# Optimization experiments

Hardware: AMD Instinct MI355X
Metric: run time of the kernel (lower is better)

Reference implementation:

```python
import jax, jax.numpy as jnp
import numpy as np

DIM = 128
HID = 128
EPS = 1e-5  # torch LayerNorm default

def _ln(x, g, b):
    mu = jnp.mean(x, axis=-1, keepdims=True)
    var = jnp.mean(jnp.square(x - mu), axis=-1, keepdims=True)
    return (x - mu) * jax.lax.rsqrt(var + EPS) * g + b

def setup_inputs() -> dict:
    key = jax.random.key(0)
    ks = jax.random.split(key, 20)
    B, N = 4, 256
    s_in = 1.0 / np.sqrt(DIM)
    s_hid = 1.0 / np.sqrt(HID)
    inp = {
        "x": jax.random.normal(ks[0], (B, N, N, DIM), jnp.float32),
        "norm_g": jnp.ones((DIM,), jnp.float32),
        "norm_b": jnp.zeros((DIM,), jnp.float32),
        "w_left": jax.random.normal(ks[1], (DIM, HID), jnp.float32) * s_in,
        "b_left": jnp.zeros((HID,), jnp.float32),
        "w_right": jax.random.normal(ks[2], (DIM, HID), jnp.float32) * s_in,
        "b_right": jnp.zeros((HID,), jnp.float32),
        # gates: module inits weight=0, bias=1; use small random weights + bias=1
        # so gradients are non-degenerate while staying near the trained-init regime
        "w_lgate": jax.random.normal(ks[3], (DIM, HID), jnp.float32) * (0.02 * s_in),
        "b_lgate": jnp.ones((HID,), jnp.float32),
        "w_rgate": jax.random.normal(ks[4], (DIM, HID), jnp.float32) * (0.02 * s_in),
        "b_rgate": jnp.ones((HID,), jnp.float32),
        "w_ogate": jax.random.normal(ks[5], (DIM, HID), jnp.float32) * (0.02 * s_in),
        "b_ogate": jnp.ones((HID,), jnp.float32),
        "onorm_g": jnp.ones((HID,), jnp.float32),
        "onorm_b": jnp.zeros((HID,), jnp.float32),
        "w_out": jax.random.normal(ks[6], (HID, DIM), jnp.float32) * s_hid,
        "b_out": jnp.zeros((DIM,), jnp.float32),
    }
    return inp

def reference(x, norm_g, norm_b, w_left, b_left, w_right, b_right,
              w_lgate, b_lgate, w_rgate, b_rgate, w_ogate, b_ogate,
              onorm_g, onorm_b, w_out, b_out):
    # x: [B, N, N, DIM]
    xn = _ln(x, norm_g, norm_b)
    left = (xn @ w_left + b_left) * jax.nn.sigmoid(xn @ w_lgate + b_lgate)
    right = (xn @ w_right + b_right) * jax.nn.sigmoid(xn @ w_rgate + b_rgate)
    out_gate = jax.nn.sigmoid(xn @ w_ogate + b_ogate)
    # 'ingoing' mix: out[b,i,j,d] = sum_k left[b,k,j,d] * right[b,k,i,d]
    mixed = jnp.einsum('bkjd,bkid->bijd', left, right)
    out = _ln(mixed, onorm_g, onorm_b) * out_gate
    return out @ w_out + b_out
```

## Files before the change

### kernel.cpp

```cpp
#include <hip/hip_runtime.h>
#include <hip/hip_fp16.h>

typedef unsigned short u16;
typedef unsigned int   u32;
typedef __attribute__((ext_vector_type(8))) short short8;
typedef __attribute__((ext_vector_type(4))) float f32x4;

#define NN 256
#define DD 128

__device__ __forceinline__ u16 f2b(float f) {
    union { float f; u32 i; } v; v.f = f;
    u32 x = v.i;
    return (u16)((x + 0x7FFFu + ((x >> 16) & 1u)) >> 16);
}
__device__ __forceinline__ float b2f(u16 u) {
    union { u32 i; float f; } v; v.i = ((u32)u) << 16; return v.f;
}
__device__ __forceinline__ u32 cvtpk(float lo, float hi) {
    u32 r;
    asm("v_cvt_pk_bf16_f32 %0, %1, %2" : "=v"(r) : "v"(lo), "v"(hi));
    return r;
}
__device__ __forceinline__ float sigm(float z) { return 1.f / (1.f + __expf(-z)); }

__global__ void k_tw(const float* w0, const float* w1, const float* w2,
                     const float* w3, const float* w4, const float* w5,
                     u16* __restrict__ out) {
    int t = blockIdx.x * 256 + threadIdx.x;
    int mat = t >> 11, idx = t & 2047;
    int lane = idx & 63;
    int s    = (idx >> 6) & 3;
    int nt   = idx >> 8;
    int m = lane & 15, quad = lane >> 4;
    int h  = nt * 16 + m;
    int d0 = s * 32 + quad * 8;
    const float* src = (mat == 0) ? w0 : (mat == 1) ? w1 : (mat == 2) ? w2
                      : (mat == 3) ? w3 : (mat == 4) ? w4 : w5;
    u16 vals[8];
#pragma unroll
    for (int j = 0; j < 8; ++j) vals[j] = f2b(src[(d0 + j) * 128 + h]);
    *(uint4*)(out + (t << 3)) = *(uint4*)vals;
}

__global__ __launch_bounds__(256, 4)
void k_lngemm(const float* __restrict__ x,
              const float* __restrict__ ng,  const float* __restrict__ nb,
              const u16*   __restrict__ wT,
              const float* __restrict__ bL,  const float* __restrict__ bLG,
              const float* __restrict__ bR,  const float* __restrict__ bRG,
              const float* __restrict__ bOG,
              u16* __restrict__ lT, u16* __restrict__ rT, float* __restrict__ og)
{
    __shared__ uint4 smem4[128 * 16];
    uint4*  xs  = smem4;
    __half* ogb = (__half*)smem4;

    const int tid = threadIdx.x;
    const int bx  = blockIdx.x;
    const int b   = bx >> 9;
    const int q   = (bx >> 1) & 255;
    const int p0  = (bx & 1) * 128;

    {
        const int lr = tid >> 4;
        const int c  = tid & 15;
        float gg[8], bbv[8];
        {
            float4 g0 = *(const float4*)(ng + c * 8);
            float4 g1 = *(const float4*)(ng + c * 8 + 4);
            float4 b0 = *(const float4*)(nb + c * 8);
            float4 b1 = *(const float4*)(nb + c * 8 + 4);
            gg[0]=g0.x; gg[1]=g0.y; gg[2]=g0.z; gg[3]=g0.w;
            gg[4]=g1.x; gg[5]=g1.y; gg[6]=g1.z; gg[7]=g1.w;
            bbv[0]=b0.x; bbv[1]=b0.y; bbv[2]=b0.z; bbv[3]=b0.w;
            bbv[4]=b1.x; bbv[5]=b1.y; bbv[6]=b1.z; bbv[7]=b1.w;
        }
#pragma unroll
        for (int pass = 0; pass < 8; ++pass) {
            const int r = pass * 16 + lr;
            const long gRow = (long)((b * NN + p0 + r) * NN + q);
            float4 x0 = *(const float4*)(x + gRow * DD + c * 8);
            float4 x1 = *(const float4*)(x + gRow * DD + c * 8 + 4);
            float f[8] = {x0.x, x0.y, x0.z, x0.w, x1.x, x1.y, x1.z, x1.w};
            float s1 = 0.f, s2 = 0.f;
#pragma unroll
            for (int j = 0; j < 8; ++j) { s1 += f[j]; s2 += f[j] * f[j]; }
#pragma unroll
            for (int off = 1; off < 16; off <<= 1) {
                s1 += __shfl_xor(s1, off);
                s2 += __shfl_xor(s2, off);
            }
            const float mu = s1 * (1.f / 128.f);
            const float rs = rsqrtf(s2 * (1.f / 128.f) - mu * mu + 1e-5f);
            uint4 pk;
            pk.x = cvtpk((f[0]-mu)*rs*gg[0]+bbv[0], (f[1]-mu)*rs*gg[1]+bbv[1]);
            pk.y = cvtpk((f[2]-mu)*rs*gg[2]+bbv[2], (f[3]-mu)*rs*gg[3]+bbv[3]);
            pk.z = cvtpk((f[4]-mu)*rs*gg[4]+bbv[4], (f[5]-mu)*rs*gg[5]+bbv[5]);
            pk.w = cvtpk((f[6]-mu)*rs*gg[6]+bbv[6], (f[7]-mu)*rs*gg[7]+bbv[7]);
            xs[r * 16 + (c ^ lr)] = pk;
        }
    }
    __syncthreads();

    const int w = tid >> 6, lane = tid & 63, quad = lane >> 4, m = lane & 15;

    short8 af[2][4];
#pragma unroll
    for (int mt = 0; mt < 2; ++mt)
#pragma unroll
        for (int s = 0; s < 4; ++s) {
            const int row = w * 32 + mt * 16 + m;
            af[mt][s] = *(const short8*)(xs + row * 16 + ((s * 4 + quad) ^ m));
        }
    __syncthreads();

    const int qt = q >> 4, qm = q & 15;

#pragma unroll 2
    for (int nt = 0; nt < 8; ++nt) {
        const int h = nt * 16 + m;
        f32x4 acc[5][2];
        const f32x4 zero = {0.f, 0.f, 0.f, 0.f};
#pragma unroll
        for (int g5 = 0; g5 < 5; ++g5) { acc[g5][0] = zero; acc[g5][1] = zero; }

#pragma unroll
        for (int g5 = 0; g5 < 5; ++g5) {
            const u16* wfb = wT + ((((g5 << 3) + nt) << 2) << 9) + (lane << 3);
#pragma unroll
            for (int s = 0; s < 4; ++s) {
                short8 bf = *(const short8*)(wfb + (s << 9));
                acc[g5][0] = __builtin_amdgcn_mfma_f32_16x16x32_bf16(af[0][s], bf, acc[g5][0], 0, 0, 0);
                acc[g5][1] = __builtin_amdgcn_mfma_f32_16x16x32_bf16(af[1][s], bf, acc[g5][1], 0, 0, 0);
            }
        }
        const float vbl  = bL[h],  vblg = bLG[h];
        const float vbr  = bR[h],  vbrg = bRG[h];
        const float vbog = bOG[h];
        const long fb = ((long)(b * 128 + h) * 16 + qt) * 8;
#pragma unroll
        for (int mt = 0; mt < 2; ++mt) {
            const int pl = w * 32 + mt * 16 + quad * 4;
            float lvf[4], rvf[4];
#pragma unroll
            for (int rg = 0; rg < 4; ++rg) {
                lvf[rg] = (acc[0][mt][rg] + vbl) * sigm(acc[1][mt][rg] + vblg);
                rvf[rg] = (acc[2][mt][rg] + vbr) * sigm(acc[3][mt][rg] + vbrg);
                float ov = sigm(acc[4][mt][rg] + vbog);
                ogb[(pl + rg) * 128 + h] = __float2half(ov);
            }
            uint2 lp2, rp2;
            lp2.x = cvtpk(lvf[0], lvf[1]); lp2.y = cvtpk(lvf[2], lvf[3]);
            rp2.x = cvtpk(rvf[0], rvf[1]); rp2.y = cvtpk(rvf[2], rvf[3]);
            const int pc = (p0 >> 5) + w;
            const int pq = mt * 2 + (quad >> 1);
            const int pr = (quad & 1) * 4;
            const long off = ((fb + pc) << 9) + qm * 32 + pq * 8 + pr;
            *(uint2*)(lT + off) = lp2;
            *(uint2*)(rT + off) = rp2;
        }
    }
    __syncthreads();

    {
#pragma unroll
        for (int it = 0; it < 16; ++it) {
            const int prow = it * 8 + w * 2 + (lane >> 5);
            const int hq   = (lane & 31) * 4;
            const __half2* s2 = (const __half2*)(ogb + prow * 128 + hq);
            float2 f01 = __half22float2(s2[0]);
            float2 f23 = __half22float2(s2[1]);
            float4 o = {f01.x, f01.y, f23.x, f23.y};
            *(float4*)(og + ((long)((b * NN + p0 + prow) * NN + q)) * DD + hq) = o;
        }
    }
}

__global__ __launch_bounds__(256)
void k_mix(const u16* __restrict__ lT, const u16* __restrict__ rT,
           u16* __restrict__ mx)
{
    const int tid = threadIdx.x;
    const int bx  = blockIdx.x;
    const int bd  = bx >> 2;
    const int it  = (bx >> 1) & 1, jt = bx & 1;
    const int w = tid >> 6, lane = tid & 63, quad = lane >> 4, m = lane & 15;
    const int ib = it * 128 + (w >> 1) * 64;
    const int jb = jt * 128 + (w & 1) * 64;
    const int iqt = it * 8 + (w >> 1) * 4;
    const int jqt = jt * 8 + (w & 1) * 4;
    const int fo = m * 32 + quad * 8;

    f32x4 acc[4][4];
    const f32x4 zero = {0.f, 0.f, 0.f, 0.f};
#pragma unroll
    for (int a = 0; a < 4; ++a)
#pragma unroll
        for (int c = 0; c < 4; ++c) acc[a][c] = zero;

#pragma unroll 1
    for (int kc = 0; kc < 8; ++kc) {
        short8 afr[4], bfr[4];
#pragma unroll
        for (int tI = 0; tI < 4; ++tI)
            afr[tI] = *(const short8*)(rT + (((long)(bd * 16 + iqt + tI) << 3) + kc) * 512 + fo);
#pragma unroll
        for (int tJ = 0; tJ < 4; ++tJ)
            bfr[tJ] = *(const short8*)(lT + (((long)(bd * 16 + jqt + tJ) << 3) + kc) * 512 + fo);
#pragma unroll
        for (int tI = 0; tI < 4; ++tI)
#pragma unroll
            for (int tJ = 0; tJ < 4; ++tJ)
                acc[tI][tJ] = __builtin_amdgcn_mfma_f32_16x16x32_bf16(bfr[tJ], afr[tI], acc[tI][tJ], 0, 0, 0);
    }

#pragma unroll
    for (int tI = 0; tI < 4; ++tI)
#pragma unroll
        for (int tJ = 0; tJ < 4; ++tJ) {
            const int i = ib + tI * 16 + m;
            const int j = jb + tJ * 16 + quad * 4;
            uint2 vv;
            vv.x = cvtpk(acc[tI][tJ][0], acc[tI][tJ][1]);
            vv.y = cvtpk(acc[tI][tJ][2], acc[tI][tJ][3]);
            *(uint2*)(mx + (long)bd * 65536 + i * 256 + j) = vv;
        }
}

__global__ __launch_bounds__(256)
void k_final(const u16* __restrict__ mx, const float* __restrict__ og,
             const u16* __restrict__ wT5, const float* __restrict__ ong,
             const float* __restrict__ onb, const float* __restrict__ bo_,
             float* __restrict__ out)
{
    __shared__ __align__(16) unsigned char smem[35328];
    uint4* m1   = (uint4*)smem;
    uint4* ys   = (uint4*)(smem + 18432);
    float* mu_s = (float*)(smem + 34816);
    float* rs_s = (float*)(smem + 35072);
    float* outs = (float*)smem;

    const int tid = threadIdx.x;
    const int bx  = blockIdx.x;
    const int b   = bx >> 10;
    const int i   = (bx >> 2) & 255;
    const int j0  = (bx & 3) * 64;
    const long base = ((long)b * 128) * 65536 + (long)i * 256 + j0;

    {
        const int dr = tid >> 3, cc = tid & 7;
#pragma unroll
        for (int pass = 0; pass < 4; ++pass) {
            const int d = pass * 32 + dr;
            m1[d * 9 + cc] = *(const uint4*)(mx + base + (long)d * 65536 + cc * 8);
        }
    }
    __syncthreads();

    if (tid < 128) {
        const int j = tid >> 1, half = tid & 1;
        float s1 = 0.f, s2 = 0.f;
        for (int d = half * 64; d < half * 64 + 64; ++d) {
            float v = b2f(((const u16*)(m1 + d * 9))[j]);
            s1 += v; s2 += v * v;
        }
        s1 += __shfl_xor(s1, 1); s2 += __shfl_xor(s2, 1);
        if (half == 0) {
            const float mu = s1 * (1.f / 128.f);
            mu_s[j] = mu;
            rs_s[j] = rsqrtf(s2 * (1.f / 128.f) - mu * mu + 1e-5f);
        }
    }
    __syncthreads();

    {
        const int j = tid >> 2, c2 = tid & 3;
        const float mu = mu_s[j], rs = rs_s[j];
        const long orow = ((long)((b * NN + i) * NN + j0 + j)) * DD;
#pragma unroll
        for (int s4 = 0; s4 < 4; ++s4) {
            const int ch = c2 * 4 + s4;
            float4 o0 = *(const float4*)(og + orow + ch * 8);
            float4 o1 = *(const float4*)(og + orow + ch * 8 + 4);
            float4 g0 = *(const float4*)(ong + ch * 8);
            float4 g1 = *(const float4*)(ong + ch * 8 + 4);
            float4 n0 = *(const float4*)(onb + ch * 8);
            float4 n1 = *(const float4*)(onb + ch * 8 + 4);
            float ov[8] = {o0.x,o0.y,o0.z,o0.w,o1.x,o1.y,o1.z,o1.w};
            float gv[8] = {g0.x,g0.y,g0.z,g0.w,g1.x,g1.y,g1.z,g1.w};
            float bv[8] = {n0.x,n0.y,n0.z,n0.w,n1.x,n1.y,n1.z,n1.w};
            float yv[8];
#pragma unroll
            for (int jj = 0; jj < 8; ++jj) {
                const int d = ch * 8 + jj;
                const float v = b2f(((const u16*)(m1 + d * 9))[j]);
                yv[jj] = ((v - mu) * rs * gv[jj] + bv[jj]) * ov[jj];
            }
            uint4 pkv;
            pkv.x = cvtpk(yv[0], yv[1]);
            pkv.y = cvtpk(yv[2], yv[3]);
            pkv.z = cvtpk(yv[4], yv[5]);
            pkv.w = cvtpk(yv[6], yv[7]);
            ys[j * 16 + (ch ^ (j & 15))] = pkv;
        }
    }
    __syncthreads();

    const int w = tid >> 6, lane = tid & 63, quad = lane >> 4, m = lane & 15;
    short8 afr[4];
#pragma unroll
    for (int s = 0; s < 4; ++s)
        afr[s] = *(const short8*)(ys + (w * 16 + m) * 16 + ((s * 4 + quad) ^ m));
    __syncthreads();

#pragma unroll 1
    for (int et = 0; et < 8; ++et) {
        f32x4 acc = {0.f, 0.f, 0.f, 0.f};
#pragma unroll
        for (int s = 0; s < 4; ++s) {
            short8 bfr = *(const short8*)(wT5 + (((et << 2) + s) << 9) + (lane << 3));
            acc = __builtin_amdgcn_mfma_f32_16x16x32_bf16(afr[s], bfr, acc, 0, 0, 0);
        }
        const int e = et * 16 + m;
        const float bo = bo_[e];
#pragma unroll
        for (int rg = 0; rg < 4; ++rg) {
            const int jl = w * 16 + quad * 4 + rg;
            outs[jl * 128 + e] = acc[rg] + bo;
        }
    }
    __syncthreads();

    {
#pragma unroll
        for (int it2 = 0; it2 < 8; ++it2) {
            const int jl = it2 * 8 + w * 2 + (lane >> 5);
            const int e4 = (lane & 31) * 4;
            float4 o = *(const float4*)(outs + jl * 128 + e4);
            *(float4*)(out + ((long)((b * NN + i) * NN + j0 + jl)) * DD + e4) = o;
        }
    }
}

extern "C" void kernel_launch(void* const* d_in, const int* in_sizes, int n_in,
                              void* d_out, int out_size, void* d_ws, size_t ws_size,
                              hipStream_t stream) {
    const float* x   = (const float*)d_in[0];
    const float* ng  = (const float*)d_in[1];
    const float* nb  = (const float*)d_in[2];
    const float* wl  = (const float*)d_in[3];
    const float* bl  = (const float*)d_in[4];
    const float* wr  = (const float*)d_in[5];
    const float* br  = (const float*)d_in[6];
    const float* wlg = (const float*)d_in[7];
    const float* blg = (const float*)d_in[8];
    const float* wrg = (const float*)d_in[9];
    const float* brg = (const float*)d_in[10];
    const float* wog = (const float*)d_in[11];
    const float* bog = (const float*)d_in[12];
    const float* ong = (const float*)d_in[13];
    const float* onb = (const float*)d_in[14];
    const float* wo  = (const float*)d_in[15];
    const float* bo  = (const float*)d_in[16];

    u16* ws = (u16*)d_ws;
    const long BIG = 33554432;
    const size_t need = (size_t)(3 * BIG + 6 * 16384) * sizeof(u16);
    if (ws_size < need) return;

    u16* lT = ws;
    u16* rT = lT + BIG;
    u16* mx = rT + BIG;
    u16* wT = mx + BIG;
    float* og = (float*)d_out;

    k_tw<<<48, 256, 0, stream>>>(wl, wlg, wr, wrg, wog, wo, wT);
    k_lngemm<<<2048, 256, 0, stream>>>(x, ng, nb, wT, bl, blg, br, brg, bog, lT, rT, og);
    k_mix<<<2048, 256, 0, stream>>>(lT, rT, mx);
    k_final<<<4096, 256, 0, stream>>>(mx, og, wT + 5 * 16384, ong, onb, bo, (float*)d_out);
}
```

Before: 519.2 us.

## Store out-gate as fp16 and stage mix output through LDS for coalesced writes

```diff
diff --git a/kernel.cpp b/kernel.cpp
--- a/kernel.cpp
+++ b/kernel.cpp
@@ -50,7 +50,7 @@
               const float* __restrict__ bL,  const float* __restrict__ bLG,
               const float* __restrict__ bR,  const float* __restrict__ bRG,
               const float* __restrict__ bOG,
-              u16* __restrict__ lT, u16* __restrict__ rT, float* __restrict__ og)
+              u16* __restrict__ lT, u16* __restrict__ rT, u16* __restrict__ ogu)
 {
     __shared__ uint4 smem4[128 * 16];
     uint4*  xs  = smem4;
@@ -63,42 +63,28 @@
     const int p0  = (bx & 1) * 128;
 
     {
-        const int lr = tid >> 4;
-        const int c  = tid & 15;
-        float gg[8], bbv[8];
-        {
-            float4 g0 = *(const float4*)(ng + c * 8);
-            float4 g1 = *(const float4*)(ng + c * 8 + 4);
-            float4 b0 = *(const float4*)(nb + c * 8);
-            float4 b1 = *(const float4*)(nb + c * 8 + 4);
-            gg[0]=g0.x; gg[1]=g0.y; gg[2]=g0.z; gg[3]=g0.w;
-            gg[4]=g1.x; gg[5]=g1.y; gg[6]=g1.z; gg[7]=g1.w;
-            bbv[0]=b0.x; bbv[1]=b0.y; bbv[2]=b0.z; bbv[3]=b0.w;
-            bbv[4]=b1.x; bbv[5]=b1.y; bbv[6]=b1.z; bbv[7]=b1.w;
-        }
-#pragma unroll
-        for (int pass = 0; pass < 8; ++pass) {
-            const int r = pass * 16 + lr;
+        const int rr = tid >> 5;
+        const int c  = tid & 31;
+        float4 gv = *(const float4*)(ng + c * 4);
+        float4 bv = *(const float4*)(nb + c * 4);
+#pragma unroll
+        for (int pass = 0; pass < 16; ++pass) {
+            const int r = pass * 8 + rr;
             const long gRow = (long)((b * NN + p0 + r) * NN + q);
-            float4 x0 = *(const float4*)(x + gRow * DD + c * 8);
-            float4 x1 = *(const float4*)(x + gRow * DD + c * 8 + 4);
-            float f[8] = {x0.x, x0.y, x0.z, x0.w, x1.x, x1.y, x1.z, x1.w};
-            float s1 = 0.f, s2 = 0.f;
-#pragma unroll
-            for (int j = 0; j < 8; ++j) { s1 += f[j]; s2 += f[j] * f[j]; }
-#pragma unroll
-            for (int off = 1; off < 16; off <<= 1) {
+            float4 xv = *(const float4*)(x + gRow * DD + c * 4);
+            float s1 = xv.x + xv.y + xv.z + xv.w;
+            float s2 = xv.x*xv.x + xv.y*xv.y + xv.z*xv.z + xv.w*xv.w;
+#pragma unroll
+            for (int off = 1; off < 32; off <<= 1) {
                 s1 += __shfl_xor(s1, off);
                 s2 += __shfl_xor(s2, off);
             }
             const float mu = s1 * (1.f / 128.f);
             const float rs = rsqrtf(s2 * (1.f / 128.f) - mu * mu + 1e-5f);
-            uint4 pk;
-            pk.x = cvtpk((f[0]-mu)*rs*gg[0]+bbv[0], (f[1]-mu)*rs*gg[1]+bbv[1]);
-            pk.y = cvtpk((f[2]-mu)*rs*gg[2]+bbv[2], (f[3]-mu)*rs*gg[3]+bbv[3]);
-            pk.z = cvtpk((f[4]-mu)*rs*gg[4]+bbv[4], (f[5]-mu)*rs*gg[5]+bbv[5]);
-            pk.w = cvtpk((f[6]-mu)*rs*gg[6]+bbv[6], (f[7]-mu)*rs*gg[7]+bbv[7]);
-            xs[r * 16 + (c ^ lr)] = pk;
+            uint2 pk;
+            pk.x = cvtpk((xv.x-mu)*rs*gv.x+bv.x, (xv.y-mu)*rs*gv.y+bv.y);
+            pk.y = cvtpk((xv.z-mu)*rs*gv.z+bv.z, (xv.w-mu)*rs*gv.w+bv.w);
+            ((uint2*)xs)[(r * 16 + ((c >> 1) ^ (r & 15))) * 2 + (c & 1)] = pk;
         }
     }
     __syncthreads();
@@ -168,11 +154,8 @@
         for (int it = 0; it < 16; ++it) {
             const int prow = it * 8 + w * 2 + (lane >> 5);
             const int hq   = (lane & 31) * 4;
-            const __half2* s2 = (const __half2*)(ogb + prow * 128 + hq);
-            float2 f01 = __half22float2(s2[0]);
-            float2 f23 = __half22float2(s2[1]);
-            float4 o = {f01.x, f01.y, f23.x, f23.y};
-            *(float4*)(og + ((long)((b * NN + p0 + prow) * NN + q)) * DD + hq) = o;
+            uint2 o = *(const uint2*)(ogb + prow * 128 + hq);
+            *(uint2*)(ogu + ((long)((b * NN + p0 + prow) * NN + q)) * 256 + hq) = o;
         }
     }
 }
@@ -181,13 +164,14 @@
 void k_mix(const u16* __restrict__ lT, const u16* __restrict__ rT,
            u16* __restrict__ mx)
 {
+    __shared__ u16 Cs[128 * 128];
     const int tid = threadIdx.x;
     const int bx  = blockIdx.x;
     const int bd  = bx >> 2;
     const int it  = (bx >> 1) & 1, jt = bx & 1;
     const int w = tid >> 6, lane = tid & 63, quad = lane >> 4, m = lane & 15;
-    const int ib = it * 128 + (w >> 1) * 64;
-    const int jb = jt * 128 + (w & 1) * 64;
+    const int iwl = (w >> 1) * 64;
+    const int jwl = (w & 1) * 64;
     const int iqt = it * 8 + (w >> 1) * 4;
     const int jqt = jt * 8 + (w & 1) * 4;
     const int fo = m * 32 + quad * 8;
@@ -219,17 +203,29 @@
     for (int tI = 0; tI < 4; ++tI)
 #pragma unroll
         for (int tJ = 0; tJ < 4; ++tJ) {
-            const int i = ib + tI * 16 + m;
-            const int j = jb + tJ * 16 + quad * 4;
+            const int iL = iwl + tI * 16 + m;
+            const int jL = jwl + tJ * 16 + quad * 4;
             uint2 vv;
             vv.x = cvtpk(acc[tI][tJ][0], acc[tI][tJ][1]);
             vv.y = cvtpk(acc[tI][tJ][2], acc[tI][tJ][3]);
-            *(uint2*)(mx + (long)bd * 65536 + i * 256 + j) = vv;
-        }
+            *(uint2*)(Cs + iL * 128 + (jL ^ ((iL & 7) << 3))) = vv;
+        }
+    __syncthreads();
+
+    {
+        const int ir = tid >> 5, cc = tid & 31;
+        const int ib0 = it * 128, jb0 = jt * 128;
+#pragma unroll
+        for (int pass = 0; pass < 16; ++pass) {
+            const int iL = pass * 8 + ir;
+            uint2 v = *(const uint2*)(Cs + iL * 128 + ((cc * 4) ^ ((iL & 7) << 3)));
+            *(uint2*)(mx + (long)bd * 65536 + (ib0 + iL) * 256 + jb0 + cc * 4) = v;
+        }
+    }
 }
 
 __global__ __launch_bounds__(256)
-void k_final(const u16* __restrict__ mx, const float* __restrict__ og,
+void k_final(const u16* __restrict__ mx, const u16* __restrict__ ogu,
              const u16* __restrict__ wT5, const float* __restrict__ ong,
              const float* __restrict__ onb, const float* __restrict__ bo_,
              float* __restrict__ out)
@@ -248,6 +244,16 @@
     const int j0  = (bx & 3) * 64;
     const long base = ((long)b * 128) * 65536 + (long)i * 256 + j0;
 
+    uint2 ogp[8];
+    {
+        const int rr = tid >> 5, c = tid & 31;
+#pragma unroll
+        for (int pass = 0; pass < 8; ++pass) {
+            const long r = (long)((b * NN + i) * NN + j0 + pass * 8 + rr);
+            ogp[pass] = *(const uint2*)(ogu + r * 256 + c * 4);
+        }
+    }
+
     {
         const int dr = tid >> 3, cc = tid & 7;
 #pragma unroll
@@ -275,34 +281,27 @@
     __syncthreads();
 
     {
-        const int j = tid >> 2, c2 = tid & 3;
-        const float mu = mu_s[j], rs = rs_s[j];
-        const long orow = ((long)((b * NN + i) * NN + j0 + j)) * DD;
-#pragma unroll
-        for (int s4 = 0; s4 < 4; ++s4) {
-            const int ch = c2 * 4 + s4;
-            float4 o0 = *(const float4*)(og + orow + ch * 8);
-            float4 o1 = *(const float4*)(og + orow + ch * 8 + 4);
-            float4 g0 = *(const float4*)(ong + ch * 8);
-            float4 g1 = *(const float4*)(ong + ch * 8 + 4);
-            float4 n0 = *(const float4*)(onb + ch * 8);
-            float4 n1 = *(const float4*)(onb + ch * 8 + 4);
-            float ov[8] = {o0.x,o0.y,o0.z,o0.w,o1.x,o1.y,o1.z,o1.w};
-            float gv[8] = {g0.x,g0.y,g0.z,g0.w,g1.x,g1.y,g1.z,g1.w};
-            float bv[8] = {n0.x,n0.y,n0.z,n0.w,n1.x,n1.y,n1.z,n1.w};
-            float yv[8];
-#pragma unroll
-            for (int jj = 0; jj < 8; ++jj) {
-                const int d = ch * 8 + jj;
-                const float v = b2f(((const u16*)(m1 + d * 9))[j]);
-                yv[jj] = ((v - mu) * rs * gv[jj] + bv[jj]) * ov[jj];
+        const int rr = tid >> 5, c = tid & 31;
+        float4 gv4 = *(const float4*)(ong + c * 4);
+        float4 bv4 = *(const float4*)(onb + c * 4);
+        const float gvv[4] = {gv4.x, gv4.y, gv4.z, gv4.w};
+        const float bvv[4] = {bv4.x, bv4.y, bv4.z, bv4.w};
+#pragma unroll
+        for (int pass = 0; pass < 8; ++pass) {
+            const int j = pass * 8 + rr;
+            const float mu = mu_s[j], rs = rs_s[j];
+            const __half* oh = (const __half*)&ogp[pass];
+            float yv[4];
+#pragma unroll
+            for (int k = 0; k < 4; ++k) {
+                const int d = c * 4 + k;
+                const float v = b2f(((const u16*)m1)[d * 72 + j]);
+                yv[k] = ((v - mu) * rs * gvv[k] + bvv[k]) * __half2float(oh[k]);
             }
-            uint4 pkv;
-            pkv.x = cvtpk(yv[0], yv[1]);
-            pkv.y = cvtpk(yv[2], yv[3]);
-            pkv.z = cvtpk(yv[4], yv[5]);
-            pkv.w = cvtpk(yv[6], yv[7]);
-            ys[j * 16 + (ch ^ (j & 15))] = pkv;
+            uint2 pk;
+            pk.x = cvtpk(yv[0], yv[1]);
+            pk.y = cvtpk(yv[2], yv[3]);
+            ((uint2*)ys)[(j * 16 + ((c >> 1) ^ (j & 15))) * 2 + (c & 1)] = pk;
         }
     }
     __syncthreads();
@@ -373,7 +372,7 @@
     u16* rT = lT + BIG;
     u16* mx = rT + BIG;
     u16* wT = mx + BIG;
-    float* og = (float*)d_out;
+    u16* og = (u16*)d_out;
 
     k_tw<<<48, 256, 0, stream>>>(wl, wlg, wr, wrg, wog, wo, wT);
     k_lngemm<<<2048, 256, 0, stream>>>(x, ng, nb, wT, bl, blg, br, brg, bog, lT, rT, og);
```

After: 473.7 us. 1.1x faster.
